# Performance work log

Hardware: AMD Instinct MI355X
Metric: run time of the kernel (lower is better)

The kernel has to match this reference:

```python
import jax, jax.numpy as jnp
import numpy as np

D_MODEL = 512
D_STATE = 64
HEADDIM = 64
EXPAND = 2
D_CONV = 4
D_INNER = EXPAND * D_MODEL            # 1024
NHEADS = D_INNER // HEADDIM           # 16
CONV_DIM = D_INNER + 2 * D_STATE      # 1152 (x, B, C share the depthwise conv)
D_IN_PROJ = 2 * D_INNER + 2 * D_STATE + NHEADS  # z, xBC, dt
C_IN = 512


def setup_inputs() -> dict:
    key = jax.random.key(0)
    ks = jax.random.split(key, 10)
    hs = jax.random.normal(ks[0], (1, C_IN, 16, 16, 16), jnp.float32)
    return {
        "hidden_states": hs,
        # 1x1 conv projections (weight stored as (out,in))
        "proj_in_w": jax.random.normal(ks[1], (D_MODEL, C_IN), jnp.float32) / np.float32(np.sqrt(C_IN)),
        "proj_in_b": jnp.zeros((D_MODEL,), jnp.float32),
        "proj_out_w": jax.random.normal(ks[2], (C_IN, D_MODEL), jnp.float32) * jnp.float32(0.02),
        "proj_out_b": jnp.zeros((C_IN,), jnp.float32),
        # Mamba2 core params
        "in_proj_w": jax.random.normal(ks[3], (D_IN_PROJ, D_MODEL), jnp.float32) / np.float32(np.sqrt(D_MODEL)),
        "conv_w": jax.random.normal(ks[4], (CONV_DIM, D_CONV), jnp.float32) / np.float32(np.sqrt(D_CONV)),
        "conv_b": jnp.zeros((CONV_DIM,), jnp.float32),
        "dt_bias": jnp.log(jnp.expm1(jax.random.uniform(ks[5], (NHEADS,), jnp.float32, 1e-3, 0.1))),
        "A_log": jnp.log(jax.random.uniform(ks[6], (NHEADS,), jnp.float32, 1.0, 16.0)),
        "D": jnp.ones((NHEADS,), jnp.float32),
        "norm_w": jnp.ones((D_INNER,), jnp.float32),
        "out_proj_w": jax.random.normal(ks[7], (D_MODEL, D_INNER), jnp.float32) / np.float32(np.sqrt(D_INNER)),
    }


def _mamba2(x, in_proj_w, conv_w, conv_b, dt_bias, A_log, Dp, norm_w, out_proj_w):
    # x: (N, T, d_model) with N = B*H*W (independent pixel sequences over time)
    N, T, _ = x.shape
    zxbcdt = jnp.einsum('ntd,ed->nte', x, in_proj_w)  # (N,T,D_IN_PROJ)
    z = zxbcdt[..., :D_INNER]
    xBC = zxbcdt[..., D_INNER:D_INNER + CONV_DIM]
    dt = zxbcdt[..., D_INNER + CONV_DIM:]             # (N,T,NHEADS)
    # causal depthwise conv along T (kernel D_CONV, left-padded), then SiLU
    pad = jnp.pad(xBC, ((0, 0), (D_CONV - 1, 0), (0, 0)))
    xc = sum(pad[:, k:k + T, :] * conv_w[:, k] for k in range(D_CONV))
    xBC = jax.nn.silu(xc + conv_b)
    xs = xBC[..., :D_INNER].reshape(N, T, NHEADS, HEADDIM)
    Bm = xBC[..., D_INNER:D_INNER + D_STATE]          # (N,T,D_STATE), ngroups=1
    Cm = xBC[..., D_INNER + D_STATE:]                 # (N,T,D_STATE)
    dt = jax.nn.softplus(dt + dt_bias)                # (N,T,NHEADS)
    A = -jnp.exp(A_log)                               # (NHEADS,)

    def step(h, inp):
        # h: (N, NHEADS, HEADDIM, D_STATE)
        dt_t, x_t, B_t, C_t = inp
        dA = jnp.exp(dt_t * A)                        # (N,NHEADS)
        h = h * dA[:, :, None, None] + (dt_t[:, :, None] * x_t)[..., None] * B_t[:, None, None, :]
        y_t = jnp.einsum('nhps,ns->nhp', h, C_t)      # (N,NHEADS,HEADDIM)
        return h, y_t

    h0 = jnp.zeros((N, NHEADS, HEADDIM, D_STATE), x.dtype)
    _, ys = jax.lax.scan(step, h0, (dt.swapaxes(0, 1), xs.swapaxes(0, 1), Bm.swapaxes(0, 1), Cm.swapaxes(0, 1)))
    y = ys.swapaxes(0, 1) + Dp[None, None, :, None] * xs   # skip term
    # gated RMSNorm: norm(y * silu(z)) * weight
    y = y.reshape(N, T, D_INNER) * jax.nn.silu(z)
    y = y * jax.lax.rsqrt(jnp.mean(y * y, axis=-1, keepdims=True) + 1e-5) * norm_w
    return jnp.einsum('ntd,od->nto', y, out_proj_w)


def reference(hidden_states, proj_in_w, proj_in_b, proj_out_w, proj_out_b,
              in_proj_w, conv_w, conv_b, dt_bias, A_log, D, norm_w, out_proj_w):
    B, C, T, H, W = hidden_states.shape
    # proj_in: 1x1 conv over channels == per-pixel matmul
    x = jnp.einsum('bcthw,dc->bthwd', hidden_states, proj_in_w) + proj_in_b
    # (B,T,H,W,D) -> (B*H*W, T, D): each pixel becomes a temporal sequence
    x = x.transpose(0, 2, 3, 1, 4).reshape(B * H * W, T, D_MODEL)
    y = _mamba2(x, in_proj_w, conv_w, conv_b, dt_bias, A_log, D, norm_w, out_proj_w)
    y = y.reshape(B, H, W, T, D_MODEL).transpose(0, 3, 1, 2, 4)  # (B,T,H,W,D)
    out = jnp.einsum('bthwd,cd->bcthw', y, proj_out_w) + proj_out_b[None, :, None, None, None]
    return (out,)
```

## Files before the change

### kernel.cpp

```cpp
#include <hip/hip_runtime.h>
#include <hip/hip_bf16.h>
#include <math.h>

#define TT       16
#define NSEQ     256
#define TOK      4096
#define DMODEL   512
#define DINNER   1024
#define DSTATE   64
#define NHEADS   16
#define HEADDIM  64
#define CONVDIM  1152
#define DINPROJ  2192
#define DTOFF    2176
#define ZLD      2176

using bf16x8 = __attribute__((ext_vector_type(8))) short;
using f32x4  = __attribute__((ext_vector_type(4))) float;
typedef __hip_bfloat16 bf16;

__device__ __forceinline__ void gload_lds16(const void* g, void* l) {
    __builtin_amdgcn_global_load_lds(
        (const __attribute__((address_space(1))) unsigned int*)g,
        (__attribute__((address_space(3))) unsigned int*)l,
        16, 0, 0);
}

template<int NFRAG>
__device__ __forceinline__ void gemm_core(
    short* As, short* Bs,
    const bf16* __restrict__ A, const bf16* __restrict__ B,
    const float* __restrict__ bias, bf16* __restrict__ Ch,
    int bm, int bn, int K, int lda, int ldb, int ldc, int Nreal)
{
    constexpr int BN = NFRAG * 32;
    const int tid = threadIdx.x;
    const int wv = tid >> 6, ln = tid & 63;
    const int m0 = bm * 128, n0 = bn * BN;
    const int wr = wv >> 1, wc = wv & 1;
    const int lr = ln & 15, lk = (ln >> 4) * 8;

    f32x4 acc[4][NFRAG];
#pragma unroll
    for (int m = 0; m < 4; ++m)
#pragma unroll
        for (int n = 0; n < NFRAG; ++n) acc[m][n] = (f32x4){0.f, 0.f, 0.f, 0.f};

    for (int k0 = 0; k0 < K; k0 += 32) {
        __syncthreads();
#pragma unroll
        for (int r = 0; r < 2; ++r) {
            const int ofs = r * 4096 + tid * 16;
            const int row = ofs >> 6;
            const int ke  = (ofs & 63) >> 1;
            gload_lds16(A + (size_t)(m0 + row) * lda + k0 + ke, (char*)As + ofs);
        }
#pragma unroll
        for (int r = 0; r < NFRAG / 2; ++r) {
            const int ofs = r * 4096 + tid * 16;
            const int row = ofs >> 6;
            const int ke  = (ofs & 63) >> 1;
            gload_lds16(B + (size_t)(n0 + row) * ldb + k0 + ke, (char*)Bs + ofs);
        }
        __syncthreads();

        bf16x8 af[4], bfr[NFRAG];
#pragma unroll
        for (int m = 0; m < 4; ++m)
            af[m] = *(const bf16x8*)&As[(wr * 64 + m * 16 + lr) * 32 + lk];
#pragma unroll
        for (int n = 0; n < NFRAG; ++n)
            bfr[n] = *(const bf16x8*)&Bs[(wc * (BN / 2) + n * 16 + lr) * 32 + lk];
#pragma unroll
        for (int m = 0; m < 4; ++m)
#pragma unroll
            for (int n = 0; n < NFRAG; ++n)
                acc[m][n] = __builtin_amdgcn_mfma_f32_16x16x32_bf16(
                    af[m], bfr[n], acc[m][n], 0, 0, 0);
    }

    const int mBase = m0 + wr * 64, nBase = n0 + wc * (BN / 2);
    float cbv[NFRAG];
#pragma unroll
    for (int n = 0; n < NFRAG; ++n) {
        const int col = nBase + n * 16 + lr;
        cbv[n] = (bias != nullptr && col < Nreal) ? bias[col] : 0.f;
    }
#pragma unroll
    for (int m = 0; m < 4; ++m) {
#pragma unroll
        for (int j = 0; j < 4; ++j) {
            const int row = mBase + m * 16 + (ln >> 4) * 4 + j;
#pragma unroll
            for (int n = 0; n < NFRAG; ++n) {
                const int col = nBase + n * 16 + lr;
                if (col < Nreal)
                    Ch[(size_t)row * ldc + col] =
                        __float2bfloat16(acc[m][n][j] + cbv[n]);
            }
        }
    }
}

__global__ __launch_bounds__(256) void k67_gemm(
    const bf16* __restrict__ A, const bf16* __restrict__ B,
    const float* __restrict__ bias, const float* __restrict__ rs,
    float* __restrict__ Cf, int K, int lda, int ldb, int ldc)
{
    __shared__ short As[128 * 32];
    __shared__ short Bs[64 * 32];

    const int tid = threadIdx.x;
    const int wv = tid >> 6, ln = tid & 63;
    const int m0 = blockIdx.x * 128, n0 = blockIdx.y * 64;
    const int wr = wv >> 1, wc = wv & 1;
    const int lr = ln & 15, lk = (ln >> 4) * 8;

    f32x4 acc[4][2];
#pragma unroll
    for (int m = 0; m < 4; ++m)
#pragma unroll
        for (int n = 0; n < 2; ++n) acc[m][n] = (f32x4){0.f, 0.f, 0.f, 0.f};

    for (int k0 = 0; k0 < K; k0 += 32) {
        __syncthreads();
#pragma unroll
        for (int r = 0; r < 2; ++r) {
            const int ofs = r * 4096 + tid * 16;
            const int row = ofs >> 6;
            const int ke  = (ofs & 63) >> 1;
            gload_lds16(A + (size_t)(m0 + row) * lda + k0 + ke, (char*)As + ofs);
        }
        {
            const int ofs = tid * 16;
            const int row = ofs >> 6;
            const int ke  = (ofs & 63) >> 1;
            gload_lds16(B + (size_t)(n0 + row) * ldb + k0 + ke, (char*)Bs + ofs);
        }
        __syncthreads();

        bf16x8 af[4], bfr[2];
#pragma unroll
        for (int m = 0; m < 4; ++m)
            af[m] = *(const bf16x8*)&As[(wr * 64 + m * 16 + lr) * 32 + lk];
#pragma unroll
        for (int n = 0; n < 2; ++n)
            bfr[n] = *(const bf16x8*)&Bs[(wc * 32 + n * 16 + lr) * 32 + lk];
#pragma unroll
        for (int m = 0; m < 4; ++m)
#pragma unroll
            for (int n = 0; n < 2; ++n)
                acc[m][n] = __builtin_amdgcn_mfma_f32_16x16x32_bf16(
                    af[m], bfr[n], acc[m][n], 0, 0, 0);
    }

    const int mBase = m0 + wr * 64, nBase = n0 + wc * 32;
    float scn[2];
#pragma unroll
    for (int n = 0; n < 2; ++n) {
        const int col = nBase + n * 16 + lr;
        const float4 pv = *(const float4*)(rs + (size_t)col * 4);
        scn[n] = rsqrtf((pv.x + pv.y + pv.z + pv.w) * (1.f / 1024.f) + 1e-5f);
    }
#pragma unroll
    for (int m = 0; m < 4; ++m) {
#pragma unroll
        for (int j = 0; j < 4; ++j) {
            const int row = mBase + m * 16 + (ln >> 4) * 4 + j;
            const float rb = bias[row];
#pragma unroll
            for (int n = 0; n < 2; ++n) {
                const int col = nBase + n * 16 + lr;
                Cf[(size_t)row * ldc + col] = acc[m][n][j] * scn[n] + rb;
            }
        }
    }
}

#define SZ_PO  (512 * 512)
#define SZ_IP2 (ZLD * 512)
#define SZ_ALL (SZ_PO + SZ_IP2)
#define NB_WC  128
#define NB_ZB  544
#define NB_WB  768
#define NB_PT  256
#define NB_WT  512
#define NB_HT  2048
#define NB_ALL (NB_WC + NB_ZB + NB_WB + NB_PT + NB_WT + NB_HT)

__global__ __launch_bounds__(256) void prep_all(
    const float* __restrict__ pi, const float* __restrict__ po,
    const float* __restrict__ op, const float* __restrict__ ip,
    const float* __restrict__ nw, const float* __restrict__ pib,
    const float* __restrict__ hs,
    bf16* __restrict__ wpo, bf16* __restrict__ wip,
    bf16* __restrict__ wpiT, bf16* __restrict__ wopT, bf16* __restrict__ hsT,
    float* __restrict__ Wc, float* __restrict__ bc, float* __restrict__ zbias)
{
    __shared__ float smem[32 * 33];
    const int b = blockIdx.x, tid = threadIdx.x;

    if (b < NB_WC) {
        const int h = b >> 3, c0 = (b & 7) * 64;
        const int w = tid >> 6, l = tid & 63;
        const float* wdt = ip + (size_t)(DTOFF + h) * DMODEL;
        float acc = 0.f;
#pragma unroll 8
        for (int i = 0; i < 128; ++i) {
            const int d = w * 128 + i;
            acc = fmaf(wdt[d], pi[(size_t)d * DMODEL + c0 + l], acc);
        }
        smem[w * 64 + l] = acc;
        __syncthreads();
        if (tid < 64)
            Wc[(size_t)h * DMODEL + c0 + tid] =
                smem[tid] + smem[64 + tid] + smem[128 + tid] + smem[192 + tid];
        if ((b & 7) == 0) {
            float p = pib[tid] * wdt[tid] + pib[tid + 256] * wdt[tid + 256];
#pragma unroll
            for (int off = 32; off >= 1; off >>= 1) p += __shfl_xor(p, off);
            if ((tid & 63) == 0) smem[300 + (tid >> 6)] = p;
            __syncthreads();
            if (tid == 0)
                bc[h] = smem[300] + smem[301] + smem[302] + smem[303];
        }
    } else if (b < NB_WC + NB_ZB) {
        const int e = (b - NB_WC) * 4 + (tid >> 6);
        const int l = tid & 63;
        const float* row = ip + (size_t)e * DMODEL;
        float acc = 0.f;
#pragma unroll
        for (int i = 0; i < 8; ++i)
            acc = fmaf(pib[l + i * 64], row[l + i * 64], acc);
#pragma unroll
        for (int off = 32; off >= 1; off >>= 1) acc += __shfl_xor(acc, off);
        if (l == 0) zbias[e] = acc;
    } else if (b < NB_WC + NB_ZB + NB_WB) {
        const int wb = b - NB_WC - NB_ZB;
        for (int idx = wb * 256 + tid; idx < SZ_ALL; idx += NB_WB * 256) {
            if (idx < SZ_PO) {
                wpo[idx] = __float2bfloat16(po[idx]);
            } else {
                int j = idx - SZ_PO;
                wip[j] = __float2bfloat16(ip[j]);
            }
        }
    } else if (b < NB_WC + NB_ZB + NB_WB + NB_PT) {
        const int tb = b - NB_WC - NB_ZB - NB_WB;
        const int c0 = (tb & 15) * 32, d0 = (tb >> 4) * 32;
        const int tx = tid & 31, ty = tid >> 5;
#pragma unroll
        for (int i = 0; i < 4; ++i)
            smem[(ty + 8 * i) * 33 + tx] =
                pi[(size_t)(d0 + ty + 8 * i) * DMODEL + c0 + tx];
        __syncthreads();
#pragma unroll
        for (int i = 0; i < 4; ++i)
            wpiT[(size_t)(c0 + ty + 8 * i) * DMODEL + d0 + tx] =
                __float2bfloat16(smem[tx * 33 + ty + 8 * i]);
    } else if (b < NB_WC + NB_ZB + NB_WB + NB_PT + NB_WT) {
        const int tb = b - NB_WC - NB_ZB - NB_WB - NB_PT;
        const int o0 = (tb & 15) * 32, d0 = (tb >> 4) * 32;
        const int tx = tid & 31, ty = tid >> 5;
#pragma unroll
        for (int i = 0; i < 4; ++i)
            smem[(ty + 8 * i) * 33 + tx] =
                op[(size_t)(o0 + ty + 8 * i) * DINNER + d0 + tx];
        __syncthreads();
#pragma unroll
        for (int i = 0; i < 4; ++i) {
            const int d = d0 + ty + 8 * i;
            wopT[(size_t)d * DMODEL + o0 + tx] =
                __float2bfloat16(smem[tx * 33 + ty + 8 * i] * nw[d]);
        }
    } else {
        const int tb = b - NB_WC - NB_ZB - NB_WB - NB_PT - NB_WT;
        const int v0 = (tb & 127) * 32, c0 = (tb >> 7) * 32;
        const int tx = tid & 31, ty = tid >> 5;
#pragma unroll
        for (int i = 0; i < 4; ++i)
            smem[(ty + 8 * i) * 33 + tx] =
                hs[(size_t)(c0 + ty + 8 * i) * TOK + v0 + tx];
        __syncthreads();
#pragma unroll
        for (int i = 0; i < 4; ++i)
            hsT[(size_t)(v0 + ty + 8 * i) * DMODEL + c0 + tx] =
                __float2bfloat16(smem[tx * 33 + ty + 8 * i]);
    }
}

__global__ __launch_bounds__(256) void gemm_w(
    const bf16* __restrict__ wpo, const bf16* __restrict__ wopT,
    const bf16* __restrict__ wip, const bf16* __restrict__ wpiT,
    bf16* __restrict__ Wbig, bf16* __restrict__ Wfuse)
{
    __shared__ short As[128 * 32];
    __shared__ short Bs[64 * 32];
    const int b = blockIdx.x;
    if (b < 64) {
        gemm_core<2>(As, Bs, wpo, wopT, nullptr, Wbig,
                     b & 3, b >> 2, DMODEL, DMODEL, DMODEL, DINNER, DINNER);
    } else {
        const int b2 = b - 64;
        gemm_core<2>(As, Bs, wip, wpiT, nullptr, Wfuse,
                     b2 >> 3, b2 & 7, DMODEL, DMODEL, DMODEL, DMODEL, DMODEL);
    }
}

__global__ __launch_bounds__(256) void k2_dt(
    const bf16* __restrict__ hsT, const bf16* __restrict__ Wfuse,
    const float* __restrict__ zbias, const float* __restrict__ Wc,
    const float* __restrict__ bc,
    bf16* __restrict__ zb, float* __restrict__ dtf)
{
    __shared__ short As[128 * 32];
    __shared__ short Bs[128 * 32];
    const int b = blockIdx.x;
    if (b < 544) {
        gemm_core<4>(As, Bs, hsT, Wfuse, zbias, zb,
                     b & 31, b >> 5, DMODEL, DMODEL, DMODEL, ZLD, ZLD);
    } else {
        const int v = b - 544;
        const int w = threadIdx.x >> 6, l = threadIdx.x & 63;
        const bf16x8 hv = *(const bf16x8*)(hsT + (size_t)v * DMODEL + l * 8);
        float hf[8];
#pragma unroll
        for (int j = 0; j < 8; ++j) {
            const unsigned int bits = ((unsigned int)(unsigned short)hv[j]) << 16;
            hf[j] = __uint_as_float(bits);
        }
#pragma unroll
        for (int hh = 0; hh < 4; ++hh) {
            const int h = w * 4 + hh;
            const float4* wr = (const float4*)(Wc + (size_t)h * DMODEL);
            const float4 w0 = wr[l * 2], w1 = wr[l * 2 + 1];
            float dot = hf[0] * w0.x + hf[1] * w0.y + hf[2] * w0.z + hf[3] * w0.w
                      + hf[4] * w1.x + hf[5] * w1.y + hf[6] * w1.z + hf[7] * w1.w;
#pragma unroll
            for (int off = 32; off >= 1; off >>= 1) dot += __shfl_xor(dot, off);
            if (l == 0) dtf[(size_t)v * 16 + h] = dot + bc[h];
        }
    }
}

__global__ __launch_bounds__(256) void ssd_kernel(
    const bf16* __restrict__ zb, const float* __restrict__ dtf,
    const float* __restrict__ conv_w, const float* __restrict__ conv_b,
    const float* __restrict__ dt_bias, const float* __restrict__ A_log,
    const float* __restrict__ Dp,
    bf16* __restrict__ gb, float* __restrict__ part)
{
    const int n = blockIdx.x, hq = blockIdx.y;
    const int tid = threadIdx.x;
    const int w = tid >> 6, p = tid & 63;
    const int h = hq * 4 + w;
    const int ch = hq * 256 + tid;

    __shared__ float Bsh[16][68];
    __shared__ float Csh[16][68];
    __shared__ float Gsh[16][16];
    __shared__ float Msh[4][256];
    __shared__ float red4[16][4];

    float ld[16];
#pragma unroll
    for (int t = 0; t < 16; ++t)
        ld[t] = __bfloat162float(zb[(size_t)(t * 256 + n) * ZLD + 1024 + ch]);

    const float cw0 = conv_w[ch * 4 + 0], cw1 = conv_w[ch * 4 + 1],
                cw2 = conv_w[ch * 4 + 2], cw3 = conv_w[ch * 4 + 3];
    const float cb = conv_b[ch];
    float xs[16];
#pragma unroll
    for (int t = 0; t < 16; ++t) {
        float a = fmaf(ld[t], cw3, cb);
        if (t >= 1) a = fmaf(ld[t - 1], cw2, a);
        if (t >= 2) a = fmaf(ld[t - 2], cw1, a);
        if (t >= 3) a = fmaf(ld[t - 3], cw0, a);
        xs[t] = a / (1.f + __expf(-a));
    }

    if (tid < 128) {
        const int cc = 1024 + tid;
        const float dw0 = conv_w[cc * 4 + 0], dw1 = conv_w[cc * 4 + 1],
                    dw2 = conv_w[cc * 4 + 2], dw3 = conv_w[cc * 4 + 3];
        const float db = conv_b[cc];
        float q0 = 0.f, q1 = 0.f, q2 = 0.f;
#pragma unroll
        for (int t = 0; t < 16; ++t) {
            const float cur =
                __bfloat162float(zb[(size_t)(t * 256 + n) * ZLD + 2048 + tid]);
            float a = fmaf(cur, dw3, db);
            a = fmaf(q2, dw2, a);
            a = fmaf(q1, dw1, a);
            a = fmaf(q0, dw0, a);
            const float val = a / (1.f + __expf(-a));
            if (tid < 64) Bsh[t][tid] = val; else Csh[t][tid - 64] = val;
            q0 = q1; q1 = q2; q2 = cur;
        }
    }

    const float a_h = -__expf(A_log[h]);
    float dtv_l = 0.f;
    if (p < 16) {
        const float raw = dtf[(size_t)(p * 256 + n) * 16 + h] + dt_bias[h];
        dtv_l = (raw > 20.f) ? raw : log1pf(__expf(raw));
    }
    float cum_l = dtv_l;
#pragma unroll
    for (int off = 1; off < 16; off <<= 1) {
        const float tmp = __shfl_up(cum_l, off);
        if (p >= off) cum_l += tmp;
    }
    __syncthreads();

    {
        const int t = tid >> 4, s = tid & 15;
        float acc = 0.f;
#pragma unroll
        for (int k = 0; k < 64; ++k)
            acc = fmaf(Csh[t][k], Bsh[s][k], acc);
        Gsh[t][s] = acc;
    }
    __syncthreads();

    float dtv_all[16], cum_all[16];
#pragma unroll
    for (int t = 0; t < 16; ++t) {
        dtv_all[t] = __shfl(dtv_l, t);
        cum_all[t] = __shfl(cum_l, t);
    }
#pragma unroll
    for (int q = 0; q < 4; ++q) {
        const int idx = p * 4 + q;
        const int t = idx >> 4, s = idx & 15;
        float m = 0.f;
        if (s <= t)
            m = __expf(a_h * (cum_all[t] - cum_all[s])) * Gsh[t][s] * dtv_all[s];
        Msh[w][idx] = m;
    }

    float zl[16];
#pragma unroll
    for (int t = 0; t < 16; ++t)
        zl[t] = __bfloat162float(zb[(size_t)(t * 256 + n) * ZLD + ch]);

    const float Dh = Dp[h];
    float g[16];
#pragma unroll
    for (int t = 0; t < 16; ++t) {
        float y = 0.f;
#pragma unroll
        for (int s = 0; s <= t; ++s)
            y = fmaf(Msh[w][t * 16 + s], xs[s], y);
        y = fmaf(Dh, xs[t], y);
        g[t] = y * (zl[t] / (1.f + __expf(-zl[t])));
    }

#pragma unroll
    for (int t = 0; t < 16; ++t) {
        float ss = g[t] * g[t];
#pragma unroll
        for (int off = 32; off >= 1; off >>= 1) ss += __shfl_xor(ss, off);
        if (p == 0) red4[t][w] = ss;
        gb[(size_t)(t * 256 + n) * DINNER + ch] = __float2bfloat16(g[t]);
    }
    __syncthreads();
    if (tid < 16)
        part[(size_t)(tid * 256 + n) * 4 + hq] =
            red4[tid][0] + red4[tid][1] + red4[tid][2] + red4[tid][3];
}

extern "C" void kernel_launch(void* const* d_in, const int* in_sizes, int n_in,
                              void* d_out, int out_size, void* d_ws, size_t ws_size,
                              hipStream_t stream) {
    const float* hs         = (const float*)d_in[0];
    const float* proj_in_w  = (const float*)d_in[1];
    const float* proj_in_b  = (const float*)d_in[2];
    const float* proj_out_w = (const float*)d_in[3];
    const float* proj_out_b = (const float*)d_in[4];
    const float* in_proj_w  = (const float*)d_in[5];
    const float* conv_w     = (const float*)d_in[6];
    const float* conv_b     = (const float*)d_in[7];
    const float* dt_bias    = (const float*)d_in[8];
    const float* A_log      = (const float*)d_in[9];
    const float* Dp         = (const float*)d_in[10];
    const float* norm_w     = (const float*)d_in[11];
    const float* out_proj_w = (const float*)d_in[12];
    float* out = (float*)d_out;

    float* ws      = (float*)d_ws;
    float* dtf     = ws;
    float* part    = dtf + (size_t)TOK * 16;
    float* Wc      = part + (size_t)TOK * 4;
    float* bc      = Wc + 16 * DMODEL;
    float* zbias   = bc + 16;
    bf16*  hsT     = (bf16*)(zbias + ZLD);
    bf16*  zb      = hsT + (size_t)TOK * DMODEL;
    bf16*  gb      = zb + (size_t)TOK * ZLD;
    bf16*  wpo     = gb + (size_t)TOK * DINNER;
    bf16*  wip     = wpo + SZ_PO;
    bf16*  wopT    = wip + SZ_IP2;
    bf16*  wpiT    = wopT + (size_t)DINNER * DMODEL;
    bf16*  Wfuse   = wpiT + (size_t)DMODEL * DMODEL;
    bf16*  Wbig    = Wfuse + (size_t)ZLD * DMODEL;

    prep_all<<<NB_ALL, 256, 0, stream>>>(
        proj_in_w, proj_out_w, out_proj_w, in_proj_w, norm_w, proj_in_b, hs,
        wpo, wip, wpiT, wopT, hsT, Wc, bc, zbias);

    gemm_w<<<200, 256, 0, stream>>>(wpo, wopT, wip, wpiT, Wbig, Wfuse);

    k2_dt<<<544 + TOK, 256, 0, stream>>>(
        hsT, Wfuse, zbias, Wc, bc, zb, dtf);

    ssd_kernel<<<dim3(NSEQ, 4), 256, 0, stream>>>(
        zb, dtf, conv_w, conv_b, dt_bias, A_log, Dp, gb, part);

    k67_gemm<<<dim3(4, 64), 256, 0, stream>>>(
        Wbig, gb, proj_out_b, part, out, DINNER, DINNER, DINNER, TOK);
}
```

Measured before the change: 99.97 us.

## Fuse weight-prep GEMMs into prep kernel reading fp32 directly, drop bf16 staging

The separate weight-conversion, transpose and weight-GEMM kernel are merged into one launch. The weight-fusion GEMMs now load fp32 weights directly, converting to bf16 (and applying norm scaling) while staging into LDS, which removes the intermediate bf16 copies and one kernel launch. The dt projection blocks now handle four tokens per block, one per wave, instead of one token per block. The trade-off is slower scalar, strided B loads in the fused GEMM, and the weight GEMMs now run at the same time as the other prep blocks.

Result: faster. 97.81 us (median of 2 runs) (-2.2%).

```diff
diff --git a/kernel.cpp b/kernel.cpp
--- a/kernel.cpp
+++ b/kernel.cpp
@@ -10,7 +10,6 @@
 #define DSTATE   64
 #define NHEADS   16
 #define HEADDIM  64
-#define CONVDIM  1152
 #define DINPROJ  2192
 #define DTOFF    2176
 #define ZLD      2176
@@ -51,15 +50,13 @@
 #pragma unroll
         for (int r = 0; r < 2; ++r) {
             const int ofs = r * 4096 + tid * 16;
-            const int row = ofs >> 6;
-            const int ke  = (ofs & 63) >> 1;
+            const int row = ofs >> 6, ke = (ofs & 63) >> 1;
             gload_lds16(A + (size_t)(m0 + row) * lda + k0 + ke, (char*)As + ofs);
         }
 #pragma unroll
         for (int r = 0; r < NFRAG / 2; ++r) {
             const int ofs = r * 4096 + tid * 16;
-            const int row = ofs >> 6;
-            const int ke  = (ofs & 63) >> 1;
+            const int row = ofs >> 6, ke = (ofs & 63) >> 1;
             gload_lds16(B + (size_t)(n0 + row) * ldb + k0 + ke, (char*)Bs + ofs);
         }
         __syncthreads();
@@ -102,20 +99,22 @@
     }
 }
 
-__global__ __launch_bounds__(256) void k67_gemm(
-    const bf16* __restrict__ A, const bf16* __restrict__ B,
-    const float* __restrict__ bias, const float* __restrict__ rs,
-    float* __restrict__ Cf, int K, int lda, int ldb, int ldc)
+template<bool SCALE>
+__device__ __forceinline__ void gemm_f32t(
+    short* As, short* Bs,
+    const float* __restrict__ A, const float* __restrict__ Bsrc,
+    const float* __restrict__ scale, bf16* __restrict__ Ch,
+    int bm, int bn, int K, int lda, int ldb, int ldc)
 {
-    __shared__ short As[128 * 32];
-    __shared__ short Bs[64 * 32];
-
     const int tid = threadIdx.x;
     const int wv = tid >> 6, ln = tid & 63;
-    const int m0 = blockIdx.x * 128, n0 = blockIdx.y * 64;
+    const int m0 = bm * 128, n0 = bn * 64;
     const int wr = wv >> 1, wc = wv & 1;
     const int lr = ln & 15, lk = (ln >> 4) * 8;
 
+    const int bn_row = tid >> 2;
+    const float bscale = SCALE ? scale[n0 + bn_row] : 1.f;
+
     f32x4 acc[4][2];
 #pragma unroll
     for (int m = 0; m < 4; ++m)
@@ -124,18 +123,25 @@
 
     for (int k0 = 0; k0 < K; k0 += 32) {
         __syncthreads();
-#pragma unroll
-        for (int r = 0; r < 2; ++r) {
-            const int ofs = r * 4096 + tid * 16;
-            const int row = ofs >> 6;
-            const int ke  = (ofs & 63) >> 1;
-            gload_lds16(A + (size_t)(m0 + row) * lda + k0 + ke, (char*)As + ofs);
-        }
         {
-            const int ofs = tid * 16;
-            const int row = ofs >> 6;
-            const int ke  = (ofs & 63) >> 1;
-            gload_lds16(B + (size_t)(n0 + row) * ldb + k0 + ke, (char*)Bs + ofs);
+            const int row = tid >> 1, koff = (tid & 1) * 16;
+            const float* src = A + (size_t)(m0 + row) * lda + k0 + koff;
+#pragma unroll
+            for (int q = 0; q < 4; ++q) {
+                const float4 v = *(const float4*)(src + q * 4);
+                As[row * 32 + koff + q * 4 + 0] = (short)__bfloat16_as_ushort(__float2bfloat16(v.x));
+                As[row * 32 + koff + q * 4 + 1] = (short)__bfloat16_as_ushort(__float2bfloat16(v.y));
+                As[row * 32 + koff + q * 4 + 2] = (short)__bfloat16_as_ushort(__float2bfloat16(v.z));
+                As[row * 32 + koff + q * 4 + 3] = (short)__bfloat16_as_ushort(__float2bfloat16(v.w));
+            }
+        }
+        {
+            const int n = bn_row, koff = (tid & 3) * 8;
+#pragma unroll
+            for (int j = 0; j < 8; ++j) {
+                const float v = Bsrc[(size_t)(k0 + koff + j) * ldb + n0 + n] * bscale;
+                Bs[n * 32 + koff + j] = (short)__bfloat16_as_ushort(__float2bfloat16(v));
+            }
         }
         __syncthreads();
 
@@ -155,53 +161,48 @@
     }
 
     const int mBase = m0 + wr * 64, nBase = n0 + wc * 32;
-    float scn[2];
-#pragma unroll
-    for (int n = 0; n < 2; ++n) {
-        const int col = nBase + n * 16 + lr;
-        const float4 pv = *(const float4*)(rs + (size_t)col * 4);
-        scn[n] = rsqrtf((pv.x + pv.y + pv.z + pv.w) * (1.f / 1024.f) + 1e-5f);
-    }
 #pragma unroll
     for (int m = 0; m < 4; ++m) {
 #pragma unroll
         for (int j = 0; j < 4; ++j) {
             const int row = mBase + m * 16 + (ln >> 4) * 4 + j;
-            const float rb = bias[row];
 #pragma unroll
             for (int n = 0; n < 2; ++n) {
                 const int col = nBase + n * 16 + lr;
-                Cf[(size_t)row * ldc + col] = acc[m][n][j] * scn[n] + rb;
+                Ch[(size_t)row * ldc + col] = __float2bfloat16(acc[m][n][j]);
             }
         }
     }
 }
 
-#define SZ_PO  (512 * 512)
-#define SZ_IP2 (ZLD * 512)
-#define SZ_ALL (SZ_PO + SZ_IP2)
-#define NB_WC  128
-#define NB_ZB  544
-#define NB_WB  768
-#define NB_PT  256
-#define NB_WT  512
-#define NB_HT  2048
-#define NB_ALL (NB_WC + NB_ZB + NB_WB + NB_PT + NB_WT + NB_HT)
-
-__global__ __launch_bounds__(256) void prep_all(
+#define NB_D1  2920
+
+__global__ __launch_bounds__(256) void d1_kernel(
     const float* __restrict__ pi, const float* __restrict__ po,
     const float* __restrict__ op, const float* __restrict__ ip,
     const float* __restrict__ nw, const float* __restrict__ pib,
     const float* __restrict__ hs,
-    bf16* __restrict__ wpo, bf16* __restrict__ wip,
-    bf16* __restrict__ wpiT, bf16* __restrict__ wopT, bf16* __restrict__ hsT,
+    bf16* __restrict__ Wfuse, bf16* __restrict__ Wbig, bf16* __restrict__ hsT,
     float* __restrict__ Wc, float* __restrict__ bc, float* __restrict__ zbias)
 {
-    __shared__ float smem[32 * 33];
+    __shared__ __align__(16) char smemraw[16384];
     const int b = blockIdx.x, tid = threadIdx.x;
 
-    if (b < NB_WC) {
-        const int h = b >> 3, c0 = (b & 7) * 64;
+    if (b < 136) {
+        short* As = (short*)smemraw;
+        short* Bs = As + 4096;
+        gemm_f32t<false>(As, Bs, ip, pi, nullptr, Wfuse,
+                         b >> 3, b & 7, DMODEL, DMODEL, DMODEL, DMODEL);
+    } else if (b < 200) {
+        short* As = (short*)smemraw;
+        short* Bs = As + 4096;
+        const int u = b - 136;
+        gemm_f32t<true>(As, Bs, po, op, nw, Wbig,
+                        u & 3, u >> 2, DMODEL, DMODEL, DINNER, DINNER);
+    } else if (b < 328) {
+        float* smem = (float*)smemraw;
+        const int b2 = b - 200;
+        const int h = b2 >> 3, c0 = (b2 & 7) * 64;
         const int w = tid >> 6, l = tid & 63;
         const float* wdt = ip + (size_t)(DTOFF + h) * DMODEL;
         float acc = 0.f;
@@ -215,7 +216,7 @@
         if (tid < 64)
             Wc[(size_t)h * DMODEL + c0 + tid] =
                 smem[tid] + smem[64 + tid] + smem[128 + tid] + smem[192 + tid];
-        if ((b & 7) == 0) {
+        if ((b2 & 7) == 0) {
             float p = pib[tid] * wdt[tid] + pib[tid + 256] * wdt[tid + 256];
 #pragma unroll
             for (int off = 32; off >= 1; off >>= 1) p += __shfl_xor(p, off);
@@ -224,8 +225,8 @@
             if (tid == 0)
                 bc[h] = smem[300] + smem[301] + smem[302] + smem[303];
         }
-    } else if (b < NB_WC + NB_ZB) {
-        const int e = (b - NB_WC) * 4 + (tid >> 6);
+    } else if (b < 872) {
+        const int e = (b - 328) * 4 + (tid >> 6);
         const int l = tid & 63;
         const float* row = ip + (size_t)e * DMODEL;
         float acc = 0.f;
@@ -235,46 +236,9 @@
 #pragma unroll
         for (int off = 32; off >= 1; off >>= 1) acc += __shfl_xor(acc, off);
         if (l == 0) zbias[e] = acc;
-    } else if (b < NB_WC + NB_ZB + NB_WB) {
-        const int wb = b - NB_WC - NB_ZB;
-        for (int idx = wb * 256 + tid; idx < SZ_ALL; idx += NB_WB * 256) {
-            if (idx < SZ_PO) {
-                wpo[idx] = __float2bfloat16(po[idx]);
-            } else {
-                int j = idx - SZ_PO;
-                wip[j] = __float2bfloat16(ip[j]);
-            }
-        }
-    } else if (b < NB_WC + NB_ZB + NB_WB + NB_PT) {
-        const int tb = b - NB_WC - NB_ZB - NB_WB;
-        const int c0 = (tb & 15) * 32, d0 = (tb >> 4) * 32;
-        const int tx = tid & 31, ty = tid >> 5;
-#pragma unroll
-        for (int i = 0; i < 4; ++i)
-            smem[(ty + 8 * i) * 33 + tx] =
-                pi[(size_t)(d0 + ty + 8 * i) * DMODEL + c0 + tx];
-        __syncthreads();
-#pragma unroll
-        for (int i = 0; i < 4; ++i)
-            wpiT[(size_t)(c0 + ty + 8 * i) * DMODEL + d0 + tx] =
-                __float2bfloat16(smem[tx * 33 + ty + 8 * i]);
-    } else if (b < NB_WC + NB_ZB + NB_WB + NB_PT + NB_WT) {
-        const int tb = b - NB_WC - NB_ZB - NB_WB - NB_PT;
-        const int o0 = (tb & 15) * 32, d0 = (tb >> 4) * 32;
-        const int tx = tid & 31, ty = tid >> 5;
-#pragma unroll
-        for (int i = 0; i < 4; ++i)
-            smem[(ty + 8 * i) * 33 + tx] =
-                op[(size_t)(o0 + ty + 8 * i) * DINNER + d0 + tx];
-        __syncthreads();
-#pragma unroll
-        for (int i = 0; i < 4; ++i) {
-            const int d = d0 + ty + 8 * i;
-            wopT[(size_t)d * DMODEL + o0 + tx] =
-                __float2bfloat16(smem[tx * 33 + ty + 8 * i] * nw[d]);
-        }
     } else {
-        const int tb = b - NB_WC - NB_ZB - NB_WB - NB_PT - NB_WT;
+        float* smem = (float*)smemraw;
+        const int tb = b - 872;
         const int v0 = (tb & 127) * 32, c0 = (tb >> 7) * 32;
         const int tx = tid & 31, ty = tid >> 5;
 #pragma unroll
@@ -289,39 +253,23 @@
     }
 }
 
-__global__ __launch_bounds__(256) void gemm_w(
-    const bf16* __restrict__ wpo, const bf16* __restrict__ wopT,
-    const bf16* __restrict__ wip, const bf16* __restrict__ wpiT,
-    bf16* __restrict__ Wbig, bf16* __restrict__ Wfuse)
-{
-    __shared__ short As[128 * 32];
-    __shared__ short Bs[64 * 32];
-    const int b = blockIdx.x;
-    if (b < 64) {
-        gemm_core<2>(As, Bs, wpo, wopT, nullptr, Wbig,
-                     b & 3, b >> 2, DMODEL, DMODEL, DMODEL, DINNER, DINNER);
-    } else {
-        const int b2 = b - 64;
-        gemm_core<2>(As, Bs, wip, wpiT, nullptr, Wfuse,
-                     b2 >> 3, b2 & 7, DMODEL, DMODEL, DMODEL, DMODEL, DMODEL);
-    }
-}
-
-__global__ __launch_bounds__(256) void k2_dt(
+__global__ __launch_bounds__(256) void d2_kernel(
     const bf16* __restrict__ hsT, const bf16* __restrict__ Wfuse,
     const float* __restrict__ zbias, const float* __restrict__ Wc,
     const float* __restrict__ bc,
     bf16* __restrict__ zb, float* __restrict__ dtf)
 {
-    __shared__ short As[128 * 32];
-    __shared__ short Bs[128 * 32];
+    __shared__ __align__(16) char smemraw[16384];
     const int b = blockIdx.x;
     if (b < 544) {
+        short* As = (short*)smemraw;
+        short* Bs = As + 4096;
         gemm_core<4>(As, Bs, hsT, Wfuse, zbias, zb,
                      b & 31, b >> 5, DMODEL, DMODEL, DMODEL, ZLD, ZLD);
     } else {
-        const int v = b - 544;
-        const int w = threadIdx.x >> 6, l = threadIdx.x & 63;
+        const int tid = threadIdx.x;
+        const int w = tid >> 6, l = tid & 63;
+        const int v = (b - 544) * 4 + w;
         const bf16x8 hv = *(const bf16x8*)(hsT + (size_t)v * DMODEL + l * 8);
         float hf[8];
 #pragma unroll
@@ -330,10 +278,9 @@
             hf[j] = __uint_as_float(bits);
         }
 #pragma unroll
-        for (int hh = 0; hh < 4; ++hh) {
-            const int h = w * 4 + hh;
-            const float4* wr = (const float4*)(Wc + (size_t)h * DMODEL);
-            const float4 w0 = wr[l * 2], w1 = wr[l * 2 + 1];
+        for (int h = 0; h < 16; ++h) {
+            const float4* wr_ = (const float4*)(Wc + (size_t)h * DMODEL);
+            const float4 w0 = wr_[l * 2], w1 = wr_[l * 2 + 1];
             float dot = hf[0] * w0.x + hf[1] * w0.y + hf[2] * w0.z + hf[3] * w0.w
                       + hf[4] * w1.x + hf[5] * w1.y + hf[6] * w1.z + hf[7] * w1.w;
 #pragma unroll
@@ -469,6 +416,79 @@
     if (tid < 16)
         part[(size_t)(tid * 256 + n) * 4 + hq] =
             red4[tid][0] + red4[tid][1] + red4[tid][2] + red4[tid][3];
+}
+
+__global__ __launch_bounds__(256) void k67_gemm(
+    const bf16* __restrict__ A, const bf16* __restrict__ B,
+    const float* __restrict__ bias, const float* __restrict__ rs,
+    float* __restrict__ Cf)
+{
+    __shared__ short As[128 * 32];
+    __shared__ short Bs[64 * 32];
+
+    const int tid = threadIdx.x;
+    const int wv = tid >> 6, ln = tid & 63;
+    const int m0 = blockIdx.x * 128, n0 = blockIdx.y * 64;
+    const int wr = wv >> 1, wc = wv & 1;
+    const int lr = ln & 15, lk = (ln >> 4) * 8;
+
+    f32x4 acc[4][2];
+#pragma unroll
+    for (int m = 0; m < 4; ++m)
+#pragma unroll
+        for (int n = 0; n < 2; ++n) acc[m][n] = (f32x4){0.f, 0.f, 0.f, 0.f};
+
+    for (int k0 = 0; k0 < DINNER; k0 += 32) {
+        __syncthreads();
+#pragma unroll
+        for (int r = 0; r < 2; ++r) {
+            const int ofs = r * 4096 + tid * 16;
+            const int row = ofs >> 6, ke = (ofs & 63) >> 1;
+            gload_lds16(A + (size_t)(m0 + row) * DINNER + k0 + ke, (char*)As + ofs);
+        }
+        {
+            const int ofs = tid * 16;
+            const int row = ofs >> 6, ke = (ofs & 63) >> 1;
+            gload_lds16(B + (size_t)(n0 + row) * DINNER + k0 + ke, (char*)Bs + ofs);
+        }
+        __syncthreads();
+
+        bf16x8 af[4], bfr[2];
+#pragma unroll
+        for (int m = 0; m < 4; ++m)
+            af[m] = *(const bf16x8*)&As[(wr * 64 + m * 16 + lr) * 32 + lk];
+#pragma unroll
+        for (int n = 0; n < 2; ++n)
+            bfr[n] = *(const bf16x8*)&Bs[(wc * 32 + n * 16 + lr) * 32 + lk];
+#pragma unroll
+        for (int m = 0; m < 4; ++m)
+#pragma unroll
+            for (int n = 0; n < 2; ++n)
+                acc[m][n] = __builtin_amdgcn_mfma_f32_16x16x32_bf16(
+                    af[m], bfr[n], acc[m][n], 0, 0, 0);
+    }
+
+    const int mBase = m0 + wr * 64, nBase = n0 + wc * 32;
+    float scn[2];
+#pragma unroll
+    for (int n = 0; n < 2; ++n) {
+        const int col = nBase + n * 16 + lr;
+        const float4 pv = *(const float4*)(rs + (size_t)col * 4);
+        scn[n] = rsqrtf((pv.x + pv.y + pv.z + pv.w) * (1.f / 1024.f) + 1e-5f);
+    }
+#pragma unroll
+    for (int m = 0; m < 4; ++m) {
+#pragma unroll
+        for (int j = 0; j < 4; ++j) {
+            const int row = mBase + m * 16 + (ln >> 4) * 4 + j;
+            const float rb = bias[row];
+#pragma unroll
+            for (int n = 0; n < 2; ++n) {
+                const int col = nBase + n * 16 + lr;
+                Cf[(size_t)row * TOK + col] = acc[m][n][j] * scn[n] + rb;
+            }
+        }
+    }
 }
 
 extern "C" void kernel_launch(void* const* d_in, const int* in_sizes, int n_in,
@@ -489,34 +509,28 @@
     const float* out_proj_w = (const float*)d_in[12];
     float* out = (float*)d_out;
 
-    float* ws      = (float*)d_ws;
-    float* dtf     = ws;
-    float* part    = dtf + (size_t)TOK * 16;
-    float* Wc      = part + (size_t)TOK * 4;
-    float* bc      = Wc + 16 * DMODEL;
-    float* zbias   = bc + 16;
-    bf16*  hsT     = (bf16*)(zbias + ZLD);
-    bf16*  zb      = hsT + (size_t)TOK * DMODEL;
-    bf16*  gb      = zb + (size_t)TOK * ZLD;
-    bf16*  wpo     = gb + (size_t)TOK * DINNER;
-    bf16*  wip     = wpo + SZ_PO;
-    bf16*  wopT    = wip + SZ_IP2;
-    bf16*  wpiT    = wopT + (size_t)DINNER * DMODEL;
-    bf16*  Wfuse   = wpiT + (size_t)DMODEL * DMODEL;
-    bf16*  Wbig    = Wfuse + (size_t)ZLD * DMODEL;
-
-    prep_all<<<NB_ALL, 256, 0, stream>>>(
+    float* ws    = (float*)d_ws;
+    float* dtf   = ws;
+    float* part  = dtf + (size_t)TOK * 16;
+    float* Wc    = part + (size_t)TOK * 4;
+    float* bc    = Wc + 16 * DMODEL;
+    float* zbias = bc + 16;
+    bf16*  hsT   = (bf16*)(zbias + ZLD);
+    bf16*  zb    = hsT + (size_t)TOK * DMODEL;
+    bf16*  gb    = zb + (size_t)TOK * ZLD;
+    bf16*  Wfuse = gb + (size_t)TOK * DINNER;
+    bf16*  Wbig  = Wfuse + (size_t)ZLD * DMODEL;
+
+    d1_kernel<<<NB_D1, 256, 0, stream>>>(
         proj_in_w, proj_out_w, out_proj_w, in_proj_w, norm_w, proj_in_b, hs,
-        wpo, wip, wpiT, wopT, hsT, Wc, bc, zbias);
-
-    gemm_w<<<200, 256, 0, stream>>>(wpo, wopT, wip, wpiT, Wbig, Wfuse);
-
-    k2_dt<<<544 + TOK, 256, 0, stream>>>(
+        Wfuse, Wbig, hsT, Wc, bc, zbias);
+
+    d2_kernel<<<544 + 1024, 256, 0, stream>>>(
         hsT, Wfuse, zbias, Wc, bc, zb, dtf);
 
     ssd_kernel<<<dim3(NSEQ, 4), 256, 0, stream>>>(
         zb, dtf, conv_w, conv_b, dt_bias, A_log, Dp, gb, part);
 
     k67_gemm<<<dim3(4, 64), 256, 0, stream>>>(
-        Wbig, gb, proj_out_b, part, out, DINNER, DINNER, DINNER, TOK);
-}
+        Wbig, gb, proj_out_b, part, out);
+}
```
